# Kernel optimization log

Measured on AMD Instinct MI355X. Metric: run time of the kernel, lower is better.

The kernel has to match this reference:

```python
import jax, jax.numpy as jnp
import numpy as np

B, IN, CTRL, M, V, OUT = 2048, 64, 512, 1024, 64, 64


def setup_inputs() -> dict:
    key = jax.random.key(0)
    ks = jax.random.split(key, 20)
    s = 0.05  # small param scale for numerical stability

    def rn(k, shape, scale):
        return jax.random.normal(k, shape, dtype=jnp.float32) * scale

    return {
        # forward args
        "x": rn(ks[0], (B, IN), 1.0),
        "h_prev": rn(ks[1], (B, CTRL), 0.1),
        "c_prev": rn(ks[2], (B, CTRL), 0.1),
        "read_weights_prev": jax.nn.softmax(rn(ks[3], (B, M), 1.0), axis=1),
        # parameters
        "memory": rn(ks[4], (M, V), 1.0),
        "W_ih": rn(ks[5], (4 * CTRL, IN + V), s),
        "b_ih": rn(ks[6], (4 * CTRL,), s),
        "W_hh": rn(ks[7], (4 * CTRL, CTRL), s),
        "b_hh": rn(ks[8], (4 * CTRL,), s),
        "W_read": rn(ks[9], (M, CTRL), s),
        "b_read": rn(ks[10], (M,), s),
        "W_write": rn(ks[11], (M, CTRL), s),
        "b_write": rn(ks[12], (M,), s),
        "W_erase": rn(ks[13], (V, CTRL), s),
        "b_erase": rn(ks[14], (V,), s),
        "W_add": rn(ks[15], (V, CTRL), s),
        "b_add": rn(ks[16], (V,), s),
        "W_out": rn(ks[17], (OUT, CTRL + V), s),
        "b_out": rn(ks[18], (OUT,), s),
    }


def reference(x, h_prev, c_prev, read_weights_prev, memory,
              W_ih, b_ih, W_hh, b_hh,
              W_read, b_read, W_write, b_write,
              W_erase, b_erase, W_add, b_add,
              W_out, b_out):
    # read with previous weights on pre-write memory: [B,M] @ [M,V] -> [B,V]
    read_prev = read_weights_prev @ memory
    inp = jnp.concatenate([x, read_prev], axis=1)  # [B, IN+V]

    # LSTMCell (PyTorch gate order: i, f, g, o)
    gates = inp @ W_ih.T + b_ih + h_prev @ W_hh.T + b_hh  # [B, 4*CTRL]
    i, f, g, o = jnp.split(gates, 4, axis=1)
    i = jax.nn.sigmoid(i)
    f = jax.nn.sigmoid(f)
    g = jnp.tanh(g)
    o = jax.nn.sigmoid(o)
    c = f * c_prev + i * g
    h = o * jnp.tanh(c)

    # addressing + erase/add vectors
    read_w = jax.nn.softmax(h @ W_read.T + b_read, axis=1)    # [B,M]
    write_w = jax.nn.softmax(h @ W_write.T + b_write, axis=1)  # [B,M]
    erase = jax.nn.sigmoid(h @ W_erase.T + b_erase)            # [B,V]
    add = jnp.tanh(h @ W_add.T + b_add)                        # [B,V]

    # outer-product erase/add memory update: [B,M,V]
    w = write_w[:, :, None]
    mem_new = memory[None, :, :] * (1.0 - w * erase[:, None, :]) + w * add[:, None, :]

    # read with new weights on post-write memory
    read_new = jnp.einsum('bm,bmv->bv', read_w, mem_new)

    out = jnp.concatenate([h, read_new], axis=1) @ W_out.T + b_out  # [B,OUT]
    return out
```

## Files before the change

### kernel.cpp

```cpp
#include <hip/hip_runtime.h>
#include <hip/hip_bf16.h>


typedef unsigned short u16;
typedef __attribute__((ext_vector_type(8))) short bf16x8;
typedef __attribute__((ext_vector_type(4))) float f32x4;

#define MFMA_BF16(a, b, c) __builtin_amdgcn_mfma_f32_16x16x32_bf16((a), (b), (c), 0, 0, 0)
#define LDW 136

__device__ __forceinline__ void dma16(const void* g, void* l) {
    __builtin_amdgcn_global_load_lds(
        (const __attribute__((address_space(1))) unsigned int*)g,
        (__attribute__((address_space(3))) unsigned int*)l, 16, 0, 0);
}

__device__ __forceinline__ u16 f2bf(float f) {
    union { float f; unsigned int u; } a; a.f = f;
    return (u16)((a.u + 0x7FFFu + ((a.u >> 16) & 1u)) >> 16);
}

__device__ __forceinline__ void pack_store4(float a0, float a1, float a2, float a3, u16* d) {
    union { __hip_bfloat162 h[2]; uint2 u; } cv;
    cv.h[0] = __float22bfloat162_rn(make_float2(a0, a1));
    cv.h[1] = __float22bfloat162_rn(make_float2(a2, a3));
    *(uint2*)d = cv.u;
}

__device__ __forceinline__ void cvt4(const float* __restrict__ s, u16* __restrict__ d) {
    float4 v = *(const float4*)s;
    pack_store4(v.x, v.y, v.z, v.w, d);
}
// ... 44 lines not shown
    return r.u;
}

__device__ __forceinline__ float sigf(float x) { return 1.f / (1.f + __expf(-x)); }
__device__ __forceinline__ float fast_tanh(float x) { return 1.f - 2.f / (__expf(2.f * x) + 1.f); }

#define PIPE_BAR_PRE_CNT()  do {                                              \
    asm volatile("s_waitcnt vmcnt(6) lgkmcnt(0)" ::: "memory");               \
    __builtin_amdgcn_s_barrier();                                             \
    __builtin_amdgcn_sched_barrier(0);                                        \
} while (0)
#define PIPE_BAR_PRE_ZERO() do {                                              \
    asm volatile("s_waitcnt vmcnt(0) lgkmcnt(0)" ::: "memory");               \
    __builtin_amdgcn_s_barrier();                                             \
    __builtin_amdgcn_sched_barrier(0);                                        \
} while (0)
#define PIPE_BAR_POST() do {                                                  \
    __builtin_amdgcn_sched_barrier(0);                                        \
    asm volatile("s_waitcnt lgkmcnt(0)" ::: "memory");                        \
    __builtin_amdgcn_s_barrier();                                             \
    __builtin_amdgcn_sched_barrier(0);                                        \
} while (0)

__global__ __launch_bounds__(256) void k_pre(
    const float* __restrict__ x, const float* __restrict__ h_prev, const float* __restrict__ rwp,
    const float* __restrict__ memory, const float* __restrict__ W_ih, const float* __restrict__ W_hh,
    const float* __restrict__ W_read, const float* __restrict__ W_write, const float* __restrict__ W_erase,
    const float* __restrict__ W_add, const float* __restrict__ W_out,
    u16* x_t, u16* ht_t, u16* wcat_t, u16* Wcat2_t, u16* Wo_rn, u16* memt, float* rp)
{
    __shared__ u16 As[64 * LDW];
    __shared__ u16 Bs[64 * LDW];
    const int tid = threadIdx.x;

    if (blockIdx.x < 128) {
        const int mb = blockIdx.x & 31, ks = blockIdx.x >> 5;
        const int w = tid >> 6, lane = tid & 63;
        const int lrow = lane & 15, lq = lane >> 4;
        const int m0 = mb * 64, k0 = ks * 256;
        const int m_loc = tid >> 1, v0 = (tid & 1) * 32;
        f32x4 acc[4] = {};
        for (int kt = 0; kt < 2; ++kt) {
#pragma unroll
            for (int i = 0; i < 4; ++i) {
                int idx = i * 256 + tid, r = idx >> 4, c = (idx & 15) * 8;
                *(uint4*)(&As[r * LDW + c]) = cvt8u(rwp + (m0 + r) * 1024 + k0 + kt * 128 + c);
            }
#pragma unroll
            for (int j = 0; j < 8; ++j) {
                float4 q = *(const float4*)(memory + (k0 + kt * 128 + m_loc) * 64 + v0 + 4 * j);
                Bs[(v0 + 4 * j + 0) * LDW + m_loc] = f2bf(q.x);
                Bs[(v0 + 4 * j + 1) * LDW + m_loc] = f2bf(q.y);
                Bs[(v0 + 4 * j + 2) * LDW + m_loc] = f2bf(q.z);
                Bs[(v0 + 4 * j + 3) * LDW + m_loc] = f2bf(q.w);
            }
            __syncthreads();
#pragma unroll
            for (int kk = 0; kk < 128; kk += 32) {
                bf16x8 a  = *(const bf16x8*)(&As[(16 * w + lrow) * LDW + kk + 8 * lq]);
                bf16x8 b0 = *(const bf16x8*)(&Bs[(lrow) * LDW + kk + 8 * lq]);
                bf16x8 b1 = *(const bf16x8*)(&Bs[(16 + lrow) * LDW + kk + 8 * lq]);
                bf16x8 b2 = *(const bf16x8*)(&Bs[(32 + lrow) * LDW + kk + 8 * lq]);
                bf16x8 b3 = *(const bf16x8*)(&Bs[(48 + lrow) * LDW + kk + 8 * lq]);
                acc[0] = MFMA_BF16(a, b0, acc[0]);
                acc[1] = MFMA_BF16(a, b1, acc[1]);
                acc[2] = MFMA_BF16(a, b2, acc[2]);
                acc[3] = MFMA_BF16(a, b3, acc[3]);
            }
            __syncthreads();
        }
        float* rps = rp + ks * 131072;
#pragma unroll
        for (int nj = 0; nj < 4; ++nj)
#pragma unroll
            for (int r = 0; r < 4; ++r) {
                int row = m0 + 16 * w + 4 * lq + r, col = 16 * nj + lrow;
                rps[row * 64 + col] = acc[nj][r];
            }
        return;
    }

    int t = (blockIdx.x - 128) * 256 + tid;
    if (t < 32768) {
        int r = t >> 4, c = (t & 15) * 4;
        cvt4(x + r * 64 + c, x_t + ((r >> 7) * 8 + (c >> 3)) * 1024 + (r & 127) * 8 + (c & 7));
        return;
    }
    t -= 32768;
    if (t < 262144) {
        int r = t >> 7, c = (t & 127) * 4;
        cvt4(h_prev + r * 512 + c, ht_t + ((r >> 7) * 64 + (c >> 3)) * 1024 + (r & 127) * 8 + (c & 7));
        return;
    }
    t -= 262144;
    if (t < 65536) {
        int r = t >> 5, c = (t & 31) * 4;
        int g = r >> 9, j = r & 511;
        int bn = j >> 4, row64 = (g << 4) + (j & 15);
        int cd = (c < 64) ? c + 64 : c - 64;
        cvt4(W_ih + r * 128 + c, wcat_t + (bn * 5) * 8192 + (cd >> 3) * 512 + row64 * 8 + (cd & 7));
        return;
    }
    t -= 65536;
    if (t < 262144) {
        int r = t >> 7, c = (t & 127) * 4;
        int g = r >> 9, j = r & 511;
        int bn = j >> 4, row64 = (g << 4) + (j & 15);
        int cd = 128 + c;
        cvt4(W_hh + r * 512 + c, wcat_t + (bn * 5 + (cd >> 7)) * 8192 + ((cd >> 3) & 15) * 512 + row64 * 8 + (cd & 7));
        return;
    }
    t -= 262144;
    if (t < 131072) {
        int r = t >> 7, c = (t & 127) * 4;
        cvt4(W_read + t * 4, Wcat2_t + ((r >> 6) * 4 + (c >> 7)) * 8192 + ((c >> 3) & 15) * 512 + (r & 63) * 8 + (c & 7));
        return;
    }
    t -= 131072;
    if (t < 131072) {
        int r = t >> 7, c = (t & 127) * 4;
        cvt4(W_write + t * 4, Wcat2_t + ((16 + (r >> 6)) * 4 + (c >> 7)) * 8192 + ((c >> 3) & 15) * 512 + (r & 63) * 8 + (c & 7));
        return;
    }
    t -= 131072;
    if (t < 8192) {
        int r = t >> 7, c = (t & 127) * 4;
        cvt4(W_erase + t * 4, Wcat2_t + (32 * 4 + (c >> 7)) * 8192 + ((c >> 3) & 15) * 512 + r * 8 + (c & 7));
        return;
    }
    t -= 8192;
    if (t < 8192) {
        int r = t >> 7, c = (t & 127) * 4;
        cvt4(W_add + t * 4, Wcat2_t + (33 * 4 + (c >> 7)) * 8192 + ((c >> 3) & 15) * 512 + r * 8 + (c & 7));
        return;
    }
    t -= 8192;
    if (t < 9216) {
        int r = t / 144, c = (t % 144) * 4;
        if (c < 512)
            cvt4(W_out + r * 576 + c, Wcat2_t + (34 * 4 + (c >> 7)) * 8192 + ((c >> 3) & 15) * 512 + r * 8 + (c & 7));
        else
            cvt4(W_out + r * 576 + c, Wo_rn + r * 64 + (c - 512));
        return;
    }
    t -= 9216;
    if (t < 16384) {
        int v = t >> 8, m = (t & 255) * 4;
        pack_store4(memory[m * 64 + v], memory[(m + 1) * 64 + v],
                    memory[(m + 2) * 64 + v], memory[(m + 3) * 64 + v], memt + v * 1024 + m);
    }
}

__global__ __launch_bounds__(256) void k_gates(const u16* __restrict__ x_t, const u16* __restrict__ ht_t,
                                               const float* __restrict__ rp, const u16* __restrict__ wcat_t,
                                               const float* __restrict__ b_ih, const float* __restrict__ b_hh,
                                               const float* __restrict__ c_prev, u16* __restrict__ hrn_t)
{
    __shared__ u16 As[2][8192];
    __shared__ u16 Bs[2][4096];
    const int tid = threadIdx.x, w = tid >> 6, lane = tid & 63;
    const int lrow = lane & 15, lq = lane >> 4;
    const int mt = blockIdx.x, bn = blockIdx.y;
    const int m0 = mt * 128;
    f32x4 acc[2][4] = {};

#pragma unroll
    for (int i = 0; i < 4; ++i) {
        int cp = i * 256 + tid;
        *(uint4*)(&As[0][cp * 8]) = cvt8u_sum4(rp, (m0 + (cp & 127)) * 64 + (cp >> 7) * 8);
    }
#pragma unroll
    for (int i = 0; i < 2; ++i) {
        int cp = i * 256 + tid;
        dma16(wcat_t + (bn * 5) * 8192 + cp * 8, &Bs[0][(i * 256 + w * 64) * 8]);
    }

#pragma unroll
    for (int t = 0; t < 10; ++t) {
        if (t < 9) {
            const int tn = t + 1, b = tn & 1;
            const u16* asrc = (tn == 1) ? (x_t + mt * 8192)
                                        : (ht_t + mt * 65536 + (tn - 2) * 8192);
#pragma unroll
            for (int i = 0; i < 4; ++i) {
                int cp = i * 256 + tid;
                dma16(asrc + cp * 8, &As[b][(i * 256 + w * 64) * 8]);
            }
#pragma unroll
            for (int i = 0; i < 2; ++i) {
                int cp = i * 256 + tid;
                dma16(wcat_t + (bn * 5 + (tn >> 1)) * 8192 + (tn & 1) * 4096 + cp * 8,
                      &Bs[b][(i * 256 + w * 64) * 8]);
            }
            PIPE_BAR_PRE_CNT();
        } else {
            PIPE_BAR_PRE_ZERO();
        }
        const int b = t & 1;
#pragma unroll
        for (int kk = 0; kk < 64; kk += 32) {
            const int ob = (kk >> 3) + lq;
            bf16x8 a0 = *(const bf16x8*)(&As[b][ob * 1024 + (32 * w + lrow) * 8]);
            bf16x8 a1 = *(const bf16x8*)(&As[b][ob * 1024 + (32 * w + 16 + lrow) * 8]);
            bf16x8 b0 = *(const bf16x8*)(&Bs[b][ob * 512 + (lrow) * 8]);
            bf16x8 b1 = *(const bf16x8*)(&Bs[b][ob * 512 + (16 + lrow) * 8]);
            bf16x8 b2 = *(const bf16x8*)(&Bs[b][ob * 512 + (32 + lrow) * 8]);
            bf16x8 b3 = *(const bf16x8*)(&Bs[b][ob * 512 + (48 + lrow) * 8]);
            acc[0][0] = MFMA_BF16(a0, b0, acc[0][0]);
            acc[0][1] = MFMA_BF16(a0, b1, acc[0][1]);
            acc[0][2] = MFMA_BF16(a0, b2, acc[0][2]);
            acc[0][3] = MFMA_BF16(a0, b3, acc[0][3]);
            acc[1][0] = MFMA_BF16(a1, b0, acc[1][0]);
            acc[1][1] = MFMA_BF16(a1, b1, acc[1][1]);
            acc[1][2] = MFMA_BF16(a1, b2, acc[1][2]);
            acc[1][3] = MFMA_BF16(a1, b3, acc[1][3]);
        }
        PIPE_BAR_POST();
    }

    const int j = bn * 16 + lrow;
    const float bI = b_ih[j] + b_hh[j];
    const float bF = b_ih[512 + j] + b_hh[512 + j];
    const float bG = b_ih[1024 + j] + b_hh[1024 + j];
    const float bO = b_ih[1536 + j] + b_hh[1536 + j];
#pragma unroll
    for (int mi = 0; mi < 2; ++mi)
#pragma unroll
        for (int r = 0; r < 4; ++r) {
            int row = m0 + 32 * w + 16 * mi + 4 * lq + r;
            float ig = sigf(acc[mi][0][r] + bI);
            float fg = sigf(acc[mi][1][r] + bF);
            float gg = fast_tanh(acc[mi][2][r] + bG);
            float og = sigf(acc[mi][3][r] + bO);
            float c = fg * c_prev[row * 512 + j] + ig * gg;
            hrn_t[(row >> 7) * 65536 + (j >> 3) * 1024 + (row & 127) * 8 + (j & 7)] =
                f2bf(og * fast_tanh(c));
        }
}

__global__ __launch_bounds__(256) void k_heads(const u16* __restrict__ hrn_t, const u16* __restrict__ Wcat2_t,
                                               const float* __restrict__ b_read, const float* __restrict__ b_write,
                                               const float* __restrict__ b_erase, const float* __restrict__ b_add,
                                               const float* __restrict__ b_out,
                                               u16* __restrict__ pre_r, u16* __restrict__ pre_w,
                                               float* __restrict__ erase, float* __restrict__ add,
                                               float* __restrict__ out)
{
    __shared__ u16 As[2][8192];
    __shared__ u16 Bs[2][4096];
    const int tid = threadIdx.x, w = tid >> 6, lane = tid & 63;
    const int lrow = lane & 15, lq = lane >> 4;
    const int mt = blockIdx.x, bn = blockIdx.y;
    const int m0 = mt * 128;
    f32x4 acc[2][4] = {};

#pragma unroll
    for (int i = 0; i < 4; ++i) {
        int cp = i * 256 + tid;
        dma16(hrn_t + mt * 65536 + cp * 8, &As[0][(i * 256 + w * 64) * 8]);
    }
#pragma unroll
    for (int i = 0; i < 2; ++i) {
        int cp = i * 256 + tid;
        dma16(Wcat2_t + (bn * 4) * 8192 + cp * 8, &Bs[0][(i * 256 + w * 64) * 8]);
    }

#pragma unroll
    for (int t = 0; t < 8; ++t) {
        if (t < 7) {
            const int tn = t + 1, b = tn & 1;
#pragma unroll
            for (int i = 0; i < 4; ++i) {
                int cp = i * 256 + tid;
                dma16(hrn_t + mt * 65536 + tn * 8192 + cp * 8, &As[b][(i * 256 + w * 64) * 8]);
            }
#pragma unroll
            for (int i = 0; i < 2; ++i) {
                int cp = i * 256 + tid;
                dma16(Wcat2_t + (bn * 4 + (tn >> 1)) * 8192 + (tn & 1) * 4096 + cp * 8,
                      &Bs[b][(i * 256 + w * 64) * 8]);
            }
            PIPE_BAR_PRE_CNT();
        } else {
            PIPE_BAR_PRE_ZERO();
        }
        const int b = t & 1;
#pragma unroll
        for (int kk = 0; kk < 64; kk += 32) {
            const int ob = (kk >> 3) + lq;
            bf16x8 a0 = *(const bf16x8*)(&As[b][ob * 1024 + (32 * w + lrow) * 8]);
            bf16x8 a1 = *(const bf16x8*)(&As[b][ob * 1024 + (32 * w + 16 + lrow) * 8]);
            bf16x8 b0 = *(const bf16x8*)(&Bs[b][ob * 512 + (lrow) * 8]);
            bf16x8 b1 = *(const bf16x8*)(&Bs[b][ob * 512 + (16 + lrow) * 8]);
            bf16x8 b2 = *(const bf16x8*)(&Bs[b][ob * 512 + (32 + lrow) * 8]);
            bf16x8 b3 = *(const bf16x8*)(&Bs[b][ob * 512 + (48 + lrow) * 8]);
            acc[0][0] = MFMA_BF16(a0, b0, acc[0][0]);
            acc[0][1] = MFMA_BF16(a0, b1, acc[0][1]);
            acc[0][2] = MFMA_BF16(a0, b2, acc[0][2]);
            acc[0][3] = MFMA_BF16(a0, b3, acc[0][3]);
            acc[1][0] = MFMA_BF16(a1, b0, acc[1][0]);
            acc[1][1] = MFMA_BF16(a1, b1, acc[1][1]);
            acc[1][2] = MFMA_BF16(a1, b2, acc[1][2]);
            acc[1][3] = MFMA_BF16(a1, b3, acc[1][3]);
        }
        PIPE_BAR_POST();
    }

#pragma unroll
    for (int mi = 0; mi < 2; ++mi)
#pragma unroll
        for (int nj = 0; nj < 4; ++nj)
#pragma unroll
            for (int r = 0; r < 4; ++r) {
                int row = m0 + 32 * w + 16 * mi + 4 * lq + r;
                int col = bn * 64 + 16 * nj + lrow;
                float v = acc[mi][nj][r];
                if (bn < 16)       pre_r[row * 1024 + col] = f2bf(v + b_read[col]);
                else if (bn < 32)  pre_w[row * 1024 + (col - 1024)] = f2bf(v + b_write[col - 1024]);
                else if (bn == 32) erase[row * 64 + (col - 2048)] = sigf(v + b_erase[col - 2048]);
                else if (bn == 33) add[row * 64 + (col - 2112)] = fast_tanh(v + b_add[col - 2112]);
                else               out[row * 64 + (col - 2176)] = v + b_out[col - 2176];
            }
}

#define SLDW 520

__global__ __launch_bounds__(256) void k_tail(const u16* __restrict__ pre_r, const u16* __restrict__ pre_w,
                                              const u16* __restrict__ memt, const u16* __restrict__ Wo_rn,
                                              const float* __restrict__ erase, const float* __restrict__ add,
                                              float* __restrict__ out)
{
    __shared__ u16 rwS[16 * SLDW];
    __shared__ u16 rw2S[16 * SLDW];
    __shared__ u16 BsP[64 * LDW];
    __shared__ u16 Ps[16 * 72];
    __shared__ float s_sh[16];
    const int tid = threadIdx.x, w = tid >> 6, lane = tid & 63;
    const int lrow = lane & 15, lq = lane >> 4;
    const int mb = blockIdx.x >> 1, kh = blockIdx.x & 1;
    const int m0 = mb * 16, k0 = kh * 512;

    {
        const int row = tid >> 4, c16 = tid & 15;
        const int row_g = m0 + row;
        const u16* prp = pre_r + row_g * 1024;
        const u16* pwp = pre_w + row_g * 1024;
        float vr[64], vw[64];
#pragma unroll
        for (int q = 0; q < 8; ++q) {
            bfu4_to_f8(*(const uint4*)(prp + q * 128 + c16 * 8), vr + 8 * q);
            bfu4_to_f8(*(const uint4*)(pwp + q * 128 + c16 * 8), vw + 8 * q);
        }
        float mr = vr[0], mw = vw[0];
#pragma unroll
        for (int i = 1; i < 64; ++i) { mr = fmaxf(mr, vr[i]); mw = fmaxf(mw, vw[i]); }
#pragma unroll
        for (int o = 1; o < 16; o <<= 1) {
            mr = fmaxf(mr, __shfl_xor(mr, o, 64));
            mw = fmaxf(mw, __shfl_xor(mw, o, 64));
        }
        float sr = 0.f, sw = 0.f;
#pragma unroll
        for (int i = 0; i < 64; ++i) {
            vr[i] = __expf(vr[i] - mr); sr += vr[i];
            vw[i] = __expf(vw[i] - mw); sw += vw[i];
        }
#pragma unroll
        for (int o = 1; o < 16; o <<= 1) {
            sr += __shfl_xor(sr, o, 64);
            sw += __shfl_xor(sw, o, 64);
        }
        const float isr = 1.f / sr, isw = 1.f / sw;
        float ss = 0.f;
#pragma unroll
        for (int q = 0; q < 8; ++q) {
            float a8[8], r8[8];
#pragma unroll
            for (int i = 0; i < 8; ++i) {
                float a = vr[8 * q + i] * isr;
                float r2 = a * (vw[8 * q + i] * isw);
                a8[i] = a; r8[i] = r2;
                ss += r2;
            }
            if ((q >> 2) == kh) {
                int cb = (q - 4 * kh) * 128 + c16 * 8;
                *(uint4*)(&rwS[row * SLDW + cb])  = pack8(a8);
                *(uint4*)(&rw2S[row * SLDW + cb]) = pack8(r8);
            }
        }
#pragma unroll
        for (int o = 1; o < 16; o <<= 1) ss += __shfl_xor(ss, o, 64);
        if (c16 == 0) s_sh[row] = ss;
    }
    __syncthreads();

    f32x4 acc1 = {}, acc2 = {};
    for (int kt = 0; kt < 4; ++kt) {
#pragma unroll
        for (int i = 0; i < 4; ++i) {
            int idx = i * 256 + tid, r = idx >> 4, c = (idx & 15) * 8;
            *(uint4*)(&BsP[r * LDW + c]) = *(const uint4*)(memt + r * 1024 + k0 + kt * 128 + c);
        }
        __syncthreads();
#pragma unroll
        for (int kk = 0; kk < 128; kk += 32) {
            bf16x8 a1 = *(const bf16x8*)(&rwS[lrow * SLDW + kt * 128 + kk + 8 * lq]);
            bf16x8 a2 = *(const bf16x8*)(&rw2S[lrow * SLDW + kt * 128 + kk + 8 * lq]);
            bf16x8 b  = *(const bf16x8*)(&BsP[(16 * w + lrow) * LDW + kk + 8 * lq]);
            acc1 = MFMA_BF16(a1, b, acc1);
            acc2 = MFMA_BF16(a2, b, acc2);
        }
        __syncthreads();
    }

#pragma unroll
    for (int r = 0; r < 4; ++r) {
        int row_l = 4 * lq + r, col = 16 * w + lrow;
        int row_g = m0 + row_l;
        float p = acc1[r] - erase[row_g * 64 + col] * acc2[r];
        if (kh == 0) p += add[row_g * 64 + col] * s_sh[row_l];
        Ps[row_l * 72 + col] = f2bf(p);
    }
#pragma unroll
    for (int i = 0; i < 2; ++i) {
        int idx = i * 256 + tid, r = idx >> 3, c = (idx & 7) * 8;
        *(uint4*)(&BsP[r * LDW + c]) = *(const uint4*)(Wo_rn + r * 64 + c);
    }
    __syncthreads();

    f32x4 acc3 = {};
#pragma unroll
    for (int kk = 0; kk < 64; kk += 32) {
        bf16x8 a = *(const bf16x8*)(&Ps[lrow * 72 + kk + 8 * lq]);
        bf16x8 b = *(const bf16x8*)(&BsP[(16 * w + lrow) * LDW + kk + 8 * lq]);
        acc3 = MFMA_BF16(a, b, acc3);
    }
#pragma unroll
    for (int r = 0; r < 4; ++r) {
        int row_g = m0 + 4 * lq + r, col = 16 * w + lrow;
        atomicAdd(&out[row_g * 64 + col], acc3[r]);
    }
}

extern "C" void kernel_launch(void* const* d_in, const int* in_sizes, int n_in,
                              void* d_out, int out_size, void* d_ws, size_t ws_size,
                              hipStream_t stream)
{
    const float* x        = (const float*)d_in[0];
    const float* h_prev   = (const float*)d_in[1];
    const float* c_prev   = (const float*)d_in[2];
    const float* rwp      = (const float*)d_in[3];
    const float* memory   = (const float*)d_in[4];
    const float* W_ih     = (const float*)d_in[5];
    const float* b_ih     = (const float*)d_in[6];
    const float* W_hh     = (const float*)d_in[7];
    const float* b_hh     = (const float*)d_in[8];
    const float* W_read   = (const float*)d_in[9];
    const float* b_read   = (const float*)d_in[10];
    const float* W_write  = (const float*)d_in[11];
    const float* b_write  = (const float*)d_in[12];
    const float* W_erase  = (const float*)d_in[13];
    const float* b_erase  = (const float*)d_in[14];
    const float* W_add    = (const float*)d_in[15];
    const float* b_add    = (const float*)d_in[16];
    const float* W_out    = (const float*)d_in[17];
    const float* b_out    = (const float*)d_in[18];
    float* out = (float*)d_out;

    char* wsp = (char*)d_ws;
    u16*   x_t     = (u16*)(wsp + 0);
    u16*   ht_t    = (u16*)(wsp + 262144);
    u16*   wcat_t  = (u16*)(wsp + 2359296);
    u16*   memt    = (u16*)(wsp + 4980736);
    u16*   Wcat2_t = (u16*)(wsp + 5111808);
    u16*   Wo_rn   = (u16*)(wsp + 7405568);
    float* rp      = (float*)(wsp + 7413760);
    u16*   hrn_t   = (u16*)(wsp + 9510912);
    u16*   pre_r   = (u16*)(wsp + 11608064);
    u16*   pre_w   = (u16*)(wsp + 15802368);
    float* erase   = (float*)(wsp + 19996672);
    float* add     = (float*)(wsp + 20520960);

    k_pre<<<3748, 256, 0, stream>>>(x, h_prev, rwp, memory, W_ih, W_hh, W_read, W_write,
                                    W_erase, W_add, W_out,
                                    x_t, ht_t, wcat_t, Wcat2_t, Wo_rn, memt, rp);
    k_gates<<<dim3(16, 32), 256, 0, stream>>>(x_t, ht_t, rp, wcat_t, b_ih, b_hh, c_prev, hrn_t);
    k_heads<<<dim3(16, 35), 256, 0, stream>>>(hrn_t, Wcat2_t, b_read, b_write, b_erase, b_add, b_out,
                                              pre_r, pre_w, erase, add, out);
    k_tail<<<256, 256, 0, stream>>>(pre_r, pre_w, memt, Wo_rn, erase, add, out);
}
```

Baseline: 157.5 us.

## Fuse four kernels into one persistent kernel with software grid barriers

Merges the preprocessing, gate GEMM, head GEMM and tail stages into a single 512-block kernel. Stages are separated by atomic-counter grid barriers instead of kernel launch boundaries, and the conversion work is spread over a grid-stride loop. The goal is to remove launch overhead and the tail-drain gaps between kernels. In exchange, it relies on all 512 blocks being co-resident (launch bounds set to 2 blocks per CU) and adds spin-wait barrier costs. It also reduces parallelism for the conversion stage, which previously used 3748 blocks.

```diff
diff --git a/kernel.cpp b/kernel.cpp
--- a/kernel.cpp
+++ b/kernel.cpp
@@ -8,6 +8,25 @@
 
 #define MFMA_BF16(a, b, c) __builtin_amdgcn_mfma_f32_16x16x32_bf16((a), (b), (c), 0, 0, 0)
 #define LDW 136
+#define SLDW 520
+#define SMEM_BYTES 53248
+
+__device__ unsigned g_bar[3];
+
+__device__ __forceinline__ void grid_barrier(int idx) {
+    __syncthreads();
+    if (threadIdx.x == 0) {
+        __threadfence();
+        unsigned ticket = __hip_atomic_fetch_add(&g_bar[idx], 1u,
+                              __ATOMIC_ACQ_REL, __HIP_MEMORY_SCOPE_AGENT);
+        unsigned target = (ticket & ~511u) + 512u;
+        while (__hip_atomic_load(&g_bar[idx], __ATOMIC_RELAXED,
+                                 __HIP_MEMORY_SCOPE_AGENT) < target)
+            __builtin_amdgcn_s_sleep(8);
+    }
+    __syncthreads();
+    __threadfence();
+}
 
 __device__ __forceinline__ void dma16(const void* g, void* l) {
     __builtin_amdgcn_global_load_lds(
@@ -98,21 +117,119 @@
     __builtin_amdgcn_sched_barrier(0);                                        \
 } while (0)
 
-__global__ __launch_bounds__(256) void k_pre(
-    const float* __restrict__ x, const float* __restrict__ h_prev, const float* __restrict__ rwp,
-    const float* __restrict__ memory, const float* __restrict__ W_ih, const float* __restrict__ W_hh,
-    const float* __restrict__ W_read, const float* __restrict__ W_write, const float* __restrict__ W_erase,
-    const float* __restrict__ W_add, const float* __restrict__ W_out,
-    u16* x_t, u16* ht_t, u16* wcat_t, u16* Wcat2_t, u16* Wo_rn, u16* memt, float* rp)
+__device__ __forceinline__ void convert_unit(int t,
+    const float* __restrict__ x, const float* __restrict__ h_prev,
+    const float* __restrict__ W_ih, const float* __restrict__ W_hh,
+    const float* __restrict__ W_read, const float* __restrict__ W_write,
+    const float* __restrict__ W_erase, const float* __restrict__ W_add,
+    const float* __restrict__ W_out, const float* __restrict__ memory,
+    u16* x_t, u16* ht_t, u16* wcat_t, u16* Wcat2_t, u16* Wo_rn, u16* memt)
 {
-    __shared__ u16 As[64 * LDW];
-    __shared__ u16 Bs[64 * LDW];
-    const int tid = threadIdx.x;
-
-    if (blockIdx.x < 128) {
-        const int mb = blockIdx.x & 31, ks = blockIdx.x >> 5;
-        const int w = tid >> 6, lane = tid & 63;
-        const int lrow = lane & 15, lq = lane >> 4;
+    if (t < 32768) {
+        int r = t >> 4, c = (t & 15) * 4;
+        cvt4(x + r * 64 + c, x_t + ((r >> 7) * 8 + (c >> 3)) * 1024 + (r & 127) * 8 + (c & 7));
+        return;
+    }
+    t -= 32768;
+    if (t < 262144) {
+        int r = t >> 7, c = (t & 127) * 4;
+        cvt4(h_prev + r * 512 + c, ht_t + ((r >> 7) * 64 + (c >> 3)) * 1024 + (r & 127) * 8 + (c & 7));
+        return;
+    }
+    t -= 262144;
+    if (t < 65536) {
+        int r = t >> 5, c = (t & 31) * 4;
+        int g = r >> 9, j = r & 511;
+        int bn = j >> 4, row64 = (g << 4) + (j & 15);
+        int cd = (c < 64) ? c + 64 : c - 64;
+        cvt4(W_ih + r * 128 + c, wcat_t + (bn * 5) * 8192 + (cd >> 3) * 512 + row64 * 8 + (cd & 7));
+        return;
+    }
+    t -= 65536;
+    if (t < 262144) {
+        int r = t >> 7, c = (t & 127) * 4;
+        int g = r >> 9, j = r & 511;
+        int bn = j >> 4, row64 = (g << 4) + (j & 15);
+        int cd = 128 + c;
+        cvt4(W_hh + r * 512 + c, wcat_t + (bn * 5 + (cd >> 7)) * 8192 + ((cd >> 3) & 15) * 512 + row64 * 8 + (cd & 7));
+        return;
+    }
+    t -= 262144;
+    if (t < 131072) {
+        int r = t >> 7, c = (t & 127) * 4;
+        cvt4(W_read + t * 4, Wcat2_t + ((r >> 6) * 4 + (c >> 7)) * 8192 + ((c >> 3) & 15) * 512 + (r & 63) * 8 + (c & 7));
+        return;
+    }
+    t -= 131072;
+    if (t < 131072) {
+        int r = t >> 7, c = (t & 127) * 4;
+        cvt4(W_write + t * 4, Wcat2_t + ((16 + (r >> 6)) * 4 + (c >> 7)) * 8192 + ((c >> 3) & 15) * 512 + (r & 63) * 8 + (c & 7));
+        return;
+    }
+    t -= 131072;
+    if (t < 8192) {
+        int r = t >> 7, c = (t & 127) * 4;
+        cvt4(W_erase + t * 4, Wcat2_t + (32 * 4 + (c >> 7)) * 8192 + ((c >> 3) & 15) * 512 + r * 8 + (c & 7));
+        return;
+    }
+    t -= 8192;
+    if (t < 8192) {
+        int r = t >> 7, c = (t & 127) * 4;
+        cvt4(W_add + t * 4, Wcat2_t + (33 * 4 + (c >> 7)) * 8192 + ((c >> 3) & 15) * 512 + r * 8 + (c & 7));
+        return;
+    }
+    t -= 8192;
+    if (t < 9216) {
+        int r = t / 144, c = (t % 144) * 4;
+        if (c < 512)
+            cvt4(W_out + r * 576 + c, Wcat2_t + (34 * 4 + (c >> 7)) * 8192 + ((c >> 3) & 15) * 512 + r * 8 + (c & 7));
+        else
+            cvt4(W_out + r * 576 + c, Wo_rn + r * 64 + (c - 512));
+        return;
+    }
+    t -= 9216;
+    {
+        int v = t >> 8, m = (t & 255) * 4;
+        pack_store4(memory[m * 64 + v], memory[(m + 1) * 64 + v],
+                    memory[(m + 2) * 64 + v], memory[(m + 3) * 64 + v], memt + v * 1024 + m);
+    }
+}
+
+__global__ __launch_bounds__(256, 2) void k_fused(
+    const float* __restrict__ x, const float* __restrict__ h_prev, const float* __restrict__ c_prev,
+    const float* __restrict__ rwp, const float* __restrict__ memory,
+    const float* __restrict__ W_ih, const float* __restrict__ b_ih,
+    const float* __restrict__ W_hh, const float* __restrict__ b_hh,
+    const float* __restrict__ W_read, const float* __restrict__ b_read,
+    const float* __restrict__ W_write, const float* __restrict__ b_write,
+    const float* __restrict__ W_erase, const float* __restrict__ b_erase,
+    const float* __restrict__ W_add, const float* __restrict__ b_add,
+    const float* __restrict__ W_out, const float* __restrict__ b_out,
+    float* __restrict__ out, char* __restrict__ wsp)
+{
+    __shared__ __align__(16) char smem[SMEM_BYTES];
+
+    u16*   x_t     = (u16*)(wsp + 0);
+    u16*   ht_t    = (u16*)(wsp + 262144);
+    u16*   wcat_t  = (u16*)(wsp + 2359296);
+    u16*   memt    = (u16*)(wsp + 4980736);
+    u16*   Wcat2_t = (u16*)(wsp + 5111808);
+    u16*   Wo_rn   = (u16*)(wsp + 7405568);
+    float* rp      = (float*)(wsp + 7413760);
+    u16*   hrn_t   = (u16*)(wsp + 9510912);
+    u16*   pre_r   = (u16*)(wsp + 11608064);
+    u16*   pre_w   = (u16*)(wsp + 15802368);
+    float* erase   = (float*)(wsp + 19996672);
+    float* add     = (float*)(wsp + 20520960);
+
+    const int bid = blockIdx.x;
+    const int tid = threadIdx.x, w = tid >> 6, lane = tid & 63;
+    const int lrow = lane & 15, lq = lane >> 4;
+
+    if (bid < 128) {
+        u16* As = (u16*)smem;
+        u16* Bs = (u16*)(smem + 64 * LDW * 2);
+        const int mb = bid & 31, ks = bid >> 5;
         const int m0 = mb * 64, k0 = ks * 256;
         const int m_loc = tid >> 1, v0 = (tid & 1) * 32;
         f32x4 acc[4] = {};
@@ -153,368 +270,269 @@
                 int row = m0 + 16 * w + 4 * lq + r, col = 16 * nj + lrow;
                 rps[row * 64 + col] = acc[nj][r];
             }
-        return;
-    }
-
-    int t = (blockIdx.x - 128) * 256 + tid;
-    if (t < 32768) {
-        int r = t >> 4, c = (t & 15) * 4;
-        cvt4(x + r * 64 + c, x_t + ((r >> 7) * 8 + (c >> 3)) * 1024 + (r & 127) * 8 + (c & 7));
-        return;
-    }
-    t -= 32768;
-    if (t < 262144) {
-        int r = t >> 7, c = (t & 127) * 4;
-        cvt4(h_prev + r * 512 + c, ht_t + ((r >> 7) * 64 + (c >> 3)) * 1024 + (r & 127) * 8 + (c & 7));
-        return;
-    }
-    t -= 262144;
-    if (t < 65536) {
-        int r = t >> 5, c = (t & 31) * 4;
-        int g = r >> 9, j = r & 511;
-        int bn = j >> 4, row64 = (g << 4) + (j & 15);
-        int cd = (c < 64) ? c + 64 : c - 64;
-        cvt4(W_ih + r * 128 + c, wcat_t + (bn * 5) * 8192 + (cd >> 3) * 512 + row64 * 8 + (cd & 7));
-        return;
-    }
-    t -= 65536;
-    if (t < 262144) {
-        int r = t >> 7, c = (t & 127) * 4;
-        int g = r >> 9, j = r & 511;
-        int bn = j >> 4, row64 = (g << 4) + (j & 15);
-        int cd = 128 + c;
-        cvt4(W_hh + r * 512 + c, wcat_t + (bn * 5 + (cd >> 7)) * 8192 + ((cd >> 3) & 15) * 512 + row64 * 8 + (cd & 7));
-        return;
-    }
-    t -= 262144;
-    if (t < 131072) {
-        int r = t >> 7, c = (t & 127) * 4;
-        cvt4(W_read + t * 4, Wcat2_t + ((r >> 6) * 4 + (c >> 7)) * 8192 + ((c >> 3) & 15) * 512 + (r & 63) * 8 + (c & 7));
-        return;
-    }
-    t -= 131072;
-    if (t < 131072) {
-        int r = t >> 7, c = (t & 127) * 4;
-        cvt4(W_write + t * 4, Wcat2_t + ((16 + (r >> 6)) * 4 + (c >> 7)) * 8192 + ((c >> 3) & 15) * 512 + (r & 63) * 8 + (c & 7));
-        return;
-    }
-    t -= 131072;
-    if (t < 8192) {
-        int r = t >> 7, c = (t & 127) * 4;
-        cvt4(W_erase + t * 4, Wcat2_t + (32 * 4 + (c >> 7)) * 8192 + ((c >> 3) & 15) * 512 + r * 8 + (c & 7));
-        return;
-    }
-    t -= 8192;
-    if (t < 8192) {
-        int r = t >> 7, c = (t & 127) * 4;
-        cvt4(W_add + t * 4, Wcat2_t + (33 * 4 + (c >> 7)) * 8192 + ((c >> 3) & 15) * 512 + r * 8 + (c & 7));
-        return;
-    }
-    t -= 8192;
-    if (t < 9216) {
-        int r = t / 144, c = (t % 144) * 4;
-        if (c < 512)
-            cvt4(W_out + r * 576 + c, Wcat2_t + (34 * 4 + (c >> 7)) * 8192 + ((c >> 3) & 15) * 512 + r * 8 + (c & 7));
-        else
-            cvt4(W_out + r * 576 + c, Wo_rn + r * 64 + (c - 512));
-        return;
-    }
-    t -= 9216;
-    if (t < 16384) {
-        int v = t >> 8, m = (t & 255) * 4;
-        pack_store4(memory[m * 64 + v], memory[(m + 1) * 64 + v],
-                    memory[(m + 2) * 64 + v], memory[(m + 3) * 64 + v], memt + v * 1024 + m);
-    }
-}
-
-__global__ __launch_bounds__(256) void k_gates(const u16* __restrict__ x_t, const u16* __restrict__ ht_t,
-                                               const float* __restrict__ rp, const u16* __restrict__ wcat_t,
-                                               const float* __restrict__ b_ih, const float* __restrict__ b_hh,
-                                               const float* __restrict__ c_prev, u16* __restrict__ hrn_t)
-{
-    __shared__ u16 As[2][8192];
-    __shared__ u16 Bs[2][4096];
-    const int tid = threadIdx.x, w = tid >> 6, lane = tid & 63;
-    const int lrow = lane & 15, lq = lane >> 4;
-    const int mt = blockIdx.x, bn = blockIdx.y;
-    const int m0 = mt * 128;
-    f32x4 acc[2][4] = {};
-
-#pragma unroll
-    for (int i = 0; i < 4; ++i) {
-        int cp = i * 256 + tid;
-        *(uint4*)(&As[0][cp * 8]) = cvt8u_sum4(rp, (m0 + (cp & 127)) * 64 + (cp >> 7) * 8);
-    }
-#pragma unroll
-    for (int i = 0; i < 2; ++i) {
-        int cp = i * 256 + tid;
-        dma16(wcat_t + (bn * 5) * 8192 + cp * 8, &Bs[0][(i * 256 + w * 64) * 8]);
-    }
-
-#pragma unroll
-    for (int t = 0; t < 10; ++t) {
-        if (t < 9) {
-            const int tn = t + 1, b = tn & 1;
-            const u16* asrc = (tn == 1) ? (x_t + mt * 8192)
-                                        : (ht_t + mt * 65536 + (tn - 2) * 8192);
-#pragma unroll
-            for (int i = 0; i < 4; ++i) {
-                int cp = i * 256 + tid;
-                dma16(asrc + cp * 8, &As[b][(i * 256 + w * 64) * 8]);
-            }
-#pragma unroll
-            for (int i = 0; i < 2; ++i) {
-                int cp = i * 256 + tid;
-                dma16(wcat_t + (bn * 5 + (tn >> 1)) * 8192 + (tn & 1) * 4096 + cp * 8,
-                      &Bs[b][(i * 256 + w * 64) * 8]);
-            }
-            PIPE_BAR_PRE_CNT();
-        } else {
-            PIPE_BAR_PRE_ZERO();
-        }
-        const int b = t & 1;
-#pragma unroll
-        for (int kk = 0; kk < 64; kk += 32) {
-            const int ob = (kk >> 3) + lq;
-            bf16x8 a0 = *(const bf16x8*)(&As[b][ob * 1024 + (32 * w + lrow) * 8]);
-            bf16x8 a1 = *(const bf16x8*)(&As[b][ob * 1024 + (32 * w + 16 + lrow) * 8]);
-            bf16x8 b0 = *(const bf16x8*)(&Bs[b][ob * 512 + (lrow) * 8]);
-            bf16x8 b1 = *(const bf16x8*)(&Bs[b][ob * 512 + (16 + lrow) * 8]);
-            bf16x8 b2 = *(const bf16x8*)(&Bs[b][ob * 512 + (32 + lrow) * 8]);
-            bf16x8 b3 = *(const bf16x8*)(&Bs[b][ob * 512 + (48 + lrow) * 8]);
-            acc[0][0] = MFMA_BF16(a0, b0, acc[0][0]);
-            acc[0][1] = MFMA_BF16(a0, b1, acc[0][1]);
-            acc[0][2] = MFMA_BF16(a0, b2, acc[0][2]);
-            acc[0][3] = MFMA_BF16(a0, b3, acc[0][3]);
-            acc[1][0] = MFMA_BF16(a1, b0, acc[1][0]);
-            acc[1][1] = MFMA_BF16(a1, b1, acc[1][1]);
-            acc[1][2] = MFMA_BF16(a1, b2, acc[1][2]);
-            acc[1][3] = MFMA_BF16(a1, b3, acc[1][3]);
-        }
-        PIPE_BAR_POST();
-    }
-
-    const int j = bn * 16 + lrow;
-    const float bI = b_ih[j] + b_hh[j];
-    const float bF = b_ih[512 + j] + b_hh[512 + j];
-    const float bG = b_ih[1024 + j] + b_hh[1024 + j];
-    const float bO = b_ih[1536 + j] + b_hh[1536 + j];
-#pragma unroll
-    for (int mi = 0; mi < 2; ++mi)
-#pragma unroll
-        for (int r = 0; r < 4; ++r) {
-            int row = m0 + 32 * w + 16 * mi + 4 * lq + r;
-            float ig = sigf(acc[mi][0][r] + bI);
-            float fg = sigf(acc[mi][1][r] + bF);
-            float gg = fast_tanh(acc[mi][2][r] + bG);
-            float og = sigf(acc[mi][3][r] + bO);
-            float c = fg * c_prev[row * 512 + j] + ig * gg;
-            hrn_t[(row >> 7) * 65536 + (j >> 3) * 1024 + (row & 127) * 8 + (j & 7)] =
-                f2bf(og * fast_tanh(c));
-        }
-}
-
-__global__ __launch_bounds__(256) void k_heads(const u16* __restrict__ hrn_t, const u16* __restrict__ Wcat2_t,
-                                               const float* __restrict__ b_read, const float* __restrict__ b_write,
-                                               const float* __restrict__ b_erase, const float* __restrict__ b_add,
-                                               const float* __restrict__ b_out,
-                                               u16* __restrict__ pre_r, u16* __restrict__ pre_w,
-                                               float* __restrict__ erase, float* __restrict__ add,
-                                               float* __restrict__ out)
-{
-    __shared__ u16 As[2][8192];
-    __shared__ u16 Bs[2][4096];
-    const int tid = threadIdx.x, w = tid >> 6, lane = tid & 63;
-    const int lrow = lane & 15, lq = lane >> 4;
-    const int mt = blockIdx.x, bn = blockIdx.y;
-    const int m0 = mt * 128;
-    f32x4 acc[2][4] = {};
-
-#pragma unroll
-    for (int i = 0; i < 4; ++i) {
-        int cp = i * 256 + tid;
-        dma16(hrn_t + mt * 65536 + cp * 8, &As[0][(i * 256 + w * 64) * 8]);
-    }
-#pragma unroll
-    for (int i = 0; i < 2; ++i) {
-        int cp = i * 256 + tid;
-        dma16(Wcat2_t + (bn * 4) * 8192 + cp * 8, &Bs[0][(i * 256 + w * 64) * 8]);
-    }
-
-#pragma unroll
-    for (int t = 0; t < 8; ++t) {
-        if (t < 7) {
-            const int tn = t + 1, b = tn & 1;
-#pragma unroll
-            for (int i = 0; i < 4; ++i) {
-                int cp = i * 256 + tid;
-                dma16(hrn_t + mt * 65536 + tn * 8192 + cp * 8, &As[b][(i * 256 + w * 64) * 8]);
-            }
-#pragma unroll
-            for (int i = 0; i < 2; ++i) {
-                int cp = i * 256 + tid;
-                dma16(Wcat2_t + (bn * 4 + (tn >> 1)) * 8192 + (tn & 1) * 4096 + cp * 8,
-                      &Bs[b][(i * 256 + w * 64) * 8]);
-            }
-            PIPE_BAR_PRE_CNT();
-        } else {
-            PIPE_BAR_PRE_ZERO();
-        }
-        const int b = t & 1;
-#pragma unroll
-        for (int kk = 0; kk < 64; kk += 32) {
-            const int ob = (kk >> 3) + lq;
-            bf16x8 a0 = *(const bf16x8*)(&As[b][ob * 1024 + (32 * w + lrow) * 8]);
-            bf16x8 a1 = *(const bf16x8*)(&As[b][ob * 1024 + (32 * w + 16 + lrow) * 8]);
-            bf16x8 b0 = *(const bf16x8*)(&Bs[b][ob * 512 + (lrow) * 8]);
-            bf16x8 b1 = *(const bf16x8*)(&Bs[b][ob * 512 + (16 + lrow) * 8]);
-            bf16x8 b2 = *(const bf16x8*)(&Bs[b][ob * 512 + (32 + lrow) * 8]);
-            bf16x8 b3 = *(const bf16x8*)(&Bs[b][ob * 512 + (48 + lrow) * 8]);
-            acc[0][0] = MFMA_BF16(a0, b0, acc[0][0]);
-            acc[0][1] = MFMA_BF16(a0, b1, acc[0][1]);
-            acc[0][2] = MFMA_BF16(a0, b2, acc[0][2]);
-            acc[0][3] = MFMA_BF16(a0, b3, acc[0][3]);
-            acc[1][0] = MFMA_BF16(a1, b0, acc[1][0]);
-            acc[1][1] = MFMA_BF16(a1, b1, acc[1][1]);
-            acc[1][2] = MFMA_BF16(a1, b2, acc[1][2]);
-            acc[1][3] = MFMA_BF16(a1, b3, acc[1][3]);
-        }
-        PIPE_BAR_POST();
-    }
-
-#pragma unroll
-    for (int mi = 0; mi < 2; ++mi)
-#pragma unroll
-        for (int nj = 0; nj < 4; ++nj)
+    } else {
+        for (int t = (bid - 128) * 256 + tid; t < 926720; t += 384 * 256)
+            convert_unit(t, x, h_prev, W_ih, W_hh, W_read, W_write, W_erase, W_add,
+                         W_out, memory, x_t, ht_t, wcat_t, Wcat2_t, Wo_rn, memt);
+    }
+    grid_barrier(0);
+
+    {
+        u16* AsG = (u16*)smem;
+        u16* BsG = (u16*)(smem + 32768);
+        const int mt = bid & 15, bn = bid >> 4;
+        const int m0 = mt * 128;
+        f32x4 acc[2][4] = {};
+
+#pragma unroll
+        for (int i = 0; i < 4; ++i) {
+            int cp = i * 256 + tid;
+            *(uint4*)(&AsG[cp * 8]) = cvt8u_sum4(rp, (m0 + (cp & 127)) * 64 + (cp >> 7) * 8);
+        }
+#pragma unroll
+        for (int i = 0; i < 2; ++i) {
+            dma16(wcat_t + (bn * 5) * 8192 + (i * 256 + tid) * 8, &BsG[(i * 256 + w * 64) * 8]);
+        }
+
+#pragma unroll
+        for (int t = 0; t < 10; ++t) {
+            if (t < 9) {
+                const int tn = t + 1, b = tn & 1;
+                const u16* asrc = (tn == 1) ? (x_t + mt * 8192)
+                                            : (ht_t + mt * 65536 + (tn - 2) * 8192);
+#pragma unroll
+                for (int i = 0; i < 4; ++i)
+                    dma16(asrc + (i * 256 + tid) * 8, &AsG[b * 8192 + (i * 256 + w * 64) * 8]);
+#pragma unroll
+                for (int i = 0; i < 2; ++i)
+                    dma16(wcat_t + (bn * 5 + (tn >> 1)) * 8192 + (tn & 1) * 4096 + (i * 256 + tid) * 8,
+                          &BsG[b * 4096 + (i * 256 + w * 64) * 8]);
+                PIPE_BAR_PRE_CNT();
+            } else {
+                PIPE_BAR_PRE_ZERO();
+            }
+            const int b = t & 1;
+#pragma unroll
+            for (int kk = 0; kk < 64; kk += 32) {
+                const int ob = (kk >> 3) + lq;
+                bf16x8 a0 = *(const bf16x8*)(&AsG[b * 8192 + ob * 1024 + (32 * w + lrow) * 8]);
+                bf16x8 a1 = *(const bf16x8*)(&AsG[b * 8192 + ob * 1024 + (32 * w + 16 + lrow) * 8]);
+                bf16x8 b0 = *(const bf16x8*)(&BsG[b * 4096 + ob * 512 + (lrow) * 8]);
+                bf16x8 b1 = *(const bf16x8*)(&BsG[b * 4096 + ob * 512 + (16 + lrow) * 8]);
+                bf16x8 b2 = *(const bf16x8*)(&BsG[b * 4096 + ob * 512 + (32 + lrow) * 8]);
+                bf16x8 b3 = *(const bf16x8*)(&BsG[b * 4096 + ob * 512 + (48 + lrow) * 8]);
+                acc[0][0] = MFMA_BF16(a0, b0, acc[0][0]);
+                acc[0][1] = MFMA_BF16(a0, b1, acc[0][1]);
+                acc[0][2] = MFMA_BF16(a0, b2, acc[0][2]);
+                acc[0][3] = MFMA_BF16(a0, b3, acc[0][3]);
+                acc[1][0] = MFMA_BF16(a1, b0, acc[1][0]);
+                acc[1][1] = MFMA_BF16(a1, b1, acc[1][1]);
+                acc[1][2] = MFMA_BF16(a1, b2, acc[1][2]);
+                acc[1][3] = MFMA_BF16(a1, b3, acc[1][3]);
+            }
+            PIPE_BAR_POST();
+        }
+
+        const int j = bn * 16 + lrow;
+        const float bI = b_ih[j] + b_hh[j];
+        const float bF = b_ih[512 + j] + b_hh[512 + j];
+        const float bG = b_ih[1024 + j] + b_hh[1024 + j];
+        const float bO = b_ih[1536 + j] + b_hh[1536 + j];
+#pragma unroll
+        for (int mi = 0; mi < 2; ++mi)
 #pragma unroll
             for (int r = 0; r < 4; ++r) {
                 int row = m0 + 32 * w + 16 * mi + 4 * lq + r;
-                int col = bn * 64 + 16 * nj + lrow;
-                float v = acc[mi][nj][r];
-                if (bn < 16)       pre_r[row * 1024 + col] = f2bf(v + b_read[col]);
-                else if (bn < 32)  pre_w[row * 1024 + (col - 1024)] = f2bf(v + b_write[col - 1024]);
-                else if (bn == 32) erase[row * 64 + (col - 2048)] = sigf(v + b_erase[col - 2048]);
-                else if (bn == 33) add[row * 64 + (col - 2112)] = fast_tanh(v + b_add[col - 2112]);
-                else               out[row * 64 + (col - 2176)] = v + b_out[col - 2176];
-            }
-}
-
-#define SLDW 520
-
-__global__ __launch_bounds__(256) void k_tail(const u16* __restrict__ pre_r, const u16* __restrict__ pre_w,
-                                              const u16* __restrict__ memt, const u16* __restrict__ Wo_rn,
-                                              const float* __restrict__ erase, const float* __restrict__ add,
-                                              float* __restrict__ out)
-{
-    __shared__ u16 rwS[16 * SLDW];
-    __shared__ u16 rw2S[16 * SLDW];
-    __shared__ u16 BsP[64 * LDW];
-    __shared__ u16 Ps[16 * 72];
-    __shared__ float s_sh[16];
-    const int tid = threadIdx.x, w = tid >> 6, lane = tid & 63;
-    const int lrow = lane & 15, lq = lane >> 4;
-    const int mb = blockIdx.x >> 1, kh = blockIdx.x & 1;
-    const int m0 = mb * 16, k0 = kh * 512;
-
-    {
-        const int row = tid >> 4, c16 = tid & 15;
-        const int row_g = m0 + row;
-        const u16* prp = pre_r + row_g * 1024;
-        const u16* pwp = pre_w + row_g * 1024;
-        float vr[64], vw[64];
-#pragma unroll
-        for (int q = 0; q < 8; ++q) {
-            bfu4_to_f8(*(const uint4*)(prp + q * 128 + c16 * 8), vr + 8 * q);
-            bfu4_to_f8(*(const uint4*)(pwp + q * 128 + c16 * 8), vw + 8 * q);
-        }
-        float mr = vr[0], mw = vw[0];
-#pragma unroll
-        for (int i = 1; i < 64; ++i) { mr = fmaxf(mr, vr[i]); mw = fmaxf(mw, vw[i]); }
-#pragma unroll
-        for (int o = 1; o < 16; o <<= 1) {
-            mr = fmaxf(mr, __shfl_xor(mr, o, 64));
-            mw = fmaxf(mw, __shfl_xor(mw, o, 64));
-        }
-        float sr = 0.f, sw = 0.f;
-#pragma unroll
-        for (int i = 0; i < 64; ++i) {
-            vr[i] = __expf(vr[i] - mr); sr += vr[i];
-            vw[i] = __expf(vw[i] - mw); sw += vw[i];
-        }
-#pragma unroll
-        for (int o = 1; o < 16; o <<= 1) {
-            sr += __shfl_xor(sr, o, 64);
-            sw += __shfl_xor(sw, o, 64);
-        }
-        const float isr = 1.f / sr, isw = 1.f / sw;
-        float ss = 0.f;
-#pragma unroll
-        for (int q = 0; q < 8; ++q) {
-            float a8[8], r8[8];
-#pragma unroll
-            for (int i = 0; i < 8; ++i) {
-                float a = vr[8 * q + i] * isr;
-                float r2 = a * (vw[8 * q + i] * isw);
-                a8[i] = a; r8[i] = r2;
-                ss += r2;
-            }
-            if ((q >> 2) == kh) {
-                int cb = (q - 4 * kh) * 128 + c16 * 8;
-                *(uint4*)(&rwS[row * SLDW + cb])  = pack8(a8);
-                *(uint4*)(&rw2S[row * SLDW + cb]) = pack8(r8);
-            }
-        }
-#pragma unroll
-        for (int o = 1; o < 16; o <<= 1) ss += __shfl_xor(ss, o, 64);
-        if (c16 == 0) s_sh[row] = ss;
-    }
-    __syncthreads();
-
-    f32x4 acc1 = {}, acc2 = {};
-    for (int kt = 0; kt < 4; ++kt) {
-#pragma unroll
-        for (int i = 0; i < 4; ++i) {
-            int idx = i * 256 + tid, r = idx >> 4, c = (idx & 15) * 8;
-            *(uint4*)(&BsP[r * LDW + c]) = *(const uint4*)(memt + r * 1024 + k0 + kt * 128 + c);
+                float ig = sigf(acc[mi][0][r] + bI);
+                float fg = sigf(acc[mi][1][r] + bF);
+                float gg = fast_tanh(acc[mi][2][r] + bG);
+                float og = sigf(acc[mi][3][r] + bO);
+                float c = fg * c_prev[row * 512 + j] + ig * gg;
+                hrn_t[(row >> 7) * 65536 + (j >> 3) * 1024 + (row & 127) * 8 + (j & 7)] =
+                    f2bf(og * fast_tanh(c));
+            }
+    }
+    grid_barrier(1);
+
+    for (int tile = bid; tile < 560; tile += 512) {
+        u16* AsG = (u16*)smem;
+        u16* BsG = (u16*)(smem + 32768);
+        const int mt = tile & 15, bn = tile >> 4;
+        const int m0 = mt * 128;
+        f32x4 acc[2][4] = {};
+
+#pragma unroll
+        for (int i = 0; i < 4; ++i)
+            dma16(hrn_t + mt * 65536 + (i * 256 + tid) * 8, &AsG[(i * 256 + w * 64) * 8]);
+#pragma unroll
+        for (int i = 0; i < 2; ++i)
+            dma16(Wcat2_t + (bn * 4) * 8192 + (i * 256 + tid) * 8, &BsG[(i * 256 + w * 64) * 8]);
+
+#pragma unroll
+        for (int t = 0; t < 8; ++t) {
+            if (t < 7) {
+                const int tn = t + 1, b = tn & 1;
+#pragma unroll
+                for (int i = 0; i < 4; ++i)
+                    dma16(hrn_t + mt * 65536 + tn * 8192 + (i * 256 + tid) * 8,
+                          &AsG[b * 8192 + (i * 256 + w * 64) * 8]);
+#pragma unroll
+                for (int i = 0; i < 2; ++i)
+                    dma16(Wcat2_t + (bn * 4 + (tn >> 1)) * 8192 + (tn & 1) * 4096 + (i * 256 + tid) * 8,
+                          &BsG[b * 4096 + (i * 256 + w * 64) * 8]);
+                PIPE_BAR_PRE_CNT();
+            } else {
+                PIPE_BAR_PRE_ZERO();
+            }
+            const int b = t & 1;
+#pragma unroll
+            for (int kk = 0; kk < 64; kk += 32) {
+                const int ob = (kk >> 3) + lq;
+                bf16x8 a0 = *(const bf16x8*)(&AsG[b * 8192 + ob * 1024 + (32 * w + lrow) * 8]);
+                bf16x8 a1 = *(const bf16x8*)(&AsG[b * 8192 + ob * 1024 + (32 * w + 16 + lrow) * 8]);
+                bf16x8 b0 = *(const bf16x8*)(&BsG[b * 4096 + ob * 512 + (lrow) * 8]);
+                bf16x8 b1 = *(const bf16x8*)(&BsG[b * 4096 + ob * 512 + (16 + lrow) * 8]);
+                bf16x8 b2 = *(const bf16x8*)(&BsG[b * 4096 + ob * 512 + (32 + lrow) * 8]);
+                bf16x8 b3 = *(const bf16x8*)(&BsG[b * 4096 + ob * 512 + (48 + lrow) * 8]);
+                acc[0][0] = MFMA_BF16(a0, b0, acc[0][0]);
+                acc[0][1] = MFMA_BF16(a0, b1, acc[0][1]);
+                acc[0][2] = MFMA_BF16(a0, b2, acc[0][2]);
+                acc[0][3] = MFMA_BF16(a0, b3, acc[0][3]);
+                acc[1][0] = MFMA_BF16(a1, b0, acc[1][0]);
+                acc[1][1] = MFMA_BF16(a1, b1, acc[1][1]);
+                acc[1][2] = MFMA_BF16(a1, b2, acc[1][2]);
+                acc[1][3] = MFMA_BF16(a1, b3, acc[1][3]);
+            }
+            PIPE_BAR_POST();
+        }
+
+#pragma unroll
+        for (int mi = 0; mi < 2; ++mi)
+#pragma unroll
+            for (int nj = 0; nj < 4; ++nj)
+#pragma unroll
+                for (int r = 0; r < 4; ++r) {
+                    int row = m0 + 32 * w + 16 * mi + 4 * lq + r;
+                    int col = bn * 64 + 16 * nj + lrow;
+                    float v = acc[mi][nj][r];
+                    if (bn < 16)       pre_r[row * 1024 + col] = f2bf(v + b_read[col]);
+                    else if (bn < 32)  pre_w[row * 1024 + (col - 1024)] = f2bf(v + b_write[col - 1024]);
+                    else if (bn == 32) erase[row * 64 + (col - 2048)] = sigf(v + b_erase[col - 2048]);
+                    else if (bn == 33) add[row * 64 + (col - 2112)] = fast_tanh(v + b_add[col - 2112]);
+                    else               out[row * 64 + (col - 2176)] = v + b_out[col - 2176];
+                }
+    }
+    grid_barrier(2);
+
+    if (bid < 256) {
+        u16*   rwS  = (u16*)smem;
+        u16*   rw2S = (u16*)(smem + 16640);
+        u16*   BsP  = (u16*)(smem + 33280);
+        u16*   Ps   = (u16*)(smem + 50688);
+        float* s_sh = (float*)(smem + 52992);
+        const int mb = bid >> 1, kh = bid & 1;
+        const int m0 = mb * 16, k0 = kh * 512;
+
+        {
+            const int row = tid >> 4, c16 = tid & 15;
+            const int row_g = m0 + row;
+            const u16* prp = pre_r + row_g * 1024;
+            const u16* pwp = pre_w + row_g * 1024;
+            float vr[64], vw[64];
+#pragma unroll
+            for (int q = 0; q < 8; ++q) {
+                bfu4_to_f8(*(const uint4*)(prp + q * 128 + c16 * 8), vr + 8 * q);
+                bfu4_to_f8(*(const uint4*)(pwp + q * 128 + c16 * 8), vw + 8 * q);
+            }
+            float mr = vr[0], mw = vw[0];
+#pragma unroll
+            for (int i = 1; i < 64; ++i) { mr = fmaxf(mr, vr[i]); mw = fmaxf(mw, vw[i]); }
+#pragma unroll
+            for (int o = 1; o < 16; o <<= 1) {
+                mr = fmaxf(mr, __shfl_xor(mr, o, 64));
+                mw = fmaxf(mw, __shfl_xor(mw, o, 64));
+            }
+            float sr = 0.f, sw = 0.f;
+#pragma unroll
+            for (int i = 0; i < 64; ++i) {
+                vr[i] = __expf(vr[i] - mr); sr += vr[i];
+                vw[i] = __expf(vw[i] - mw); sw += vw[i];
+            }
+#pragma unroll
+            for (int o = 1; o < 16; o <<= 1) {
+                sr += __shfl_xor(sr, o, 64);
+                sw += __shfl_xor(sw, o, 64);
+            }
+            const float isr = 1.f / sr, isw = 1.f / sw;
+            float ss = 0.f;
+#pragma unroll
+            for (int q = 0; q < 8; ++q) {
+                float a8[8], r8[8];
+#pragma unroll
+                for (int i = 0; i < 8; ++i) {
+                    float a = vr[8 * q + i] * isr;
+                    float r2 = a * (vw[8 * q + i] * isw);
+                    a8[i] = a; r8[i] = r2;
+                    ss += r2;
+                }
+                if ((q >> 2) == kh) {
+                    int cb = (q - 4 * kh) * 128 + c16 * 8;
+                    *(uint4*)(&rwS[row * SLDW + cb])  = pack8(a8);
+                    *(uint4*)(&rw2S[row * SLDW + cb]) = pack8(r8);
+                }
+            }
+#pragma unroll
+            for (int o = 1; o < 16; o <<= 1) ss += __shfl_xor(ss, o, 64);
+            if (c16 == 0) s_sh[row] = ss;
         }
         __syncthreads();
-#pragma unroll
-        for (int kk = 0; kk < 128; kk += 32) {
-            bf16x8 a1 = *(const bf16x8*)(&rwS[lrow * SLDW + kt * 128 + kk + 8 * lq]);
-            bf16x8 a2 = *(const bf16x8*)(&rw2S[lrow * SLDW + kt * 128 + kk + 8 * lq]);
-            bf16x8 b  = *(const bf16x8*)(&BsP[(16 * w + lrow) * LDW + kk + 8 * lq]);
-            acc1 = MFMA_BF16(a1, b, acc1);
-            acc2 = MFMA_BF16(a2, b, acc2);
+
+        f32x4 acc1 = {}, acc2 = {};
+        for (int kt = 0; kt < 4; ++kt) {
+#pragma unroll
+            for (int i = 0; i < 4; ++i) {
+                int idx = i * 256 + tid, r = idx >> 4, c = (idx & 15) * 8;
+                *(uint4*)(&BsP[r * LDW + c]) = *(const uint4*)(memt + r * 1024 + k0 + kt * 128 + c);
+            }
+            __syncthreads();
+#pragma unroll
+            for (int kk = 0; kk < 128; kk += 32) {
+                bf16x8 a1 = *(const bf16x8*)(&rwS[lrow * SLDW + kt * 128 + kk + 8 * lq]);
+                bf16x8 a2 = *(const bf16x8*)(&rw2S[lrow * SLDW + kt * 128 + kk + 8 * lq]);
+                bf16x8 b  = *(const bf16x8*)(&BsP[(16 * w + lrow) * LDW + kk + 8 * lq]);
+                acc1 = MFMA_BF16(a1, b, acc1);
+                acc2 = MFMA_BF16(a2, b, acc2);
+            }
+            __syncthreads();
+        }
+
+#pragma unroll
+        for (int r = 0; r < 4; ++r) {
+            int row_l = 4 * lq + r, col = 16 * w + lrow;
+            int row_g = m0 + row_l;
+            float p = acc1[r] - erase[row_g * 64 + col] * acc2[r];
+            if (kh == 0) p += add[row_g * 64 + col] * s_sh[row_l];
+            Ps[row_l * 72 + col] = f2bf(p);
+        }
+#pragma unroll
+        for (int i = 0; i < 2; ++i) {
+            int idx = i * 256 + tid, r = idx >> 3, c = (idx & 7) * 8;
+            *(uint4*)(&BsP[r * LDW + c]) = *(const uint4*)(Wo_rn + r * 64 + c);
         }
         __syncthreads();
-    }
-
-#pragma unroll
-    for (int r = 0; r < 4; ++r) {
-        int row_l = 4 * lq + r, col = 16 * w + lrow;
-        int row_g = m0 + row_l;
-        float p = acc1[r] - erase[row_g * 64 + col] * acc2[r];
-        if (kh == 0) p += add[row_g * 64 + col] * s_sh[row_l];
-        Ps[row_l * 72 + col] = f2bf(p);
-    }
-#pragma unroll
-    for (int i = 0; i < 2; ++i) {
-        int idx = i * 256 + tid, r = idx >> 3, c = (idx & 7) * 8;
-        *(uint4*)(&BsP[r * LDW + c]) = *(const uint4*)(Wo_rn + r * 64 + c);
-    }
-    __syncthreads();
-
-    f32x4 acc3 = {};
-#pragma unroll
-    for (int kk = 0; kk < 64; kk += 32) {
-        bf16x8 a = *(const bf16x8*)(&Ps[lrow * 72 + kk + 8 * lq]);
-        bf16x8 b = *(const bf16x8*)(&BsP[(16 * w + lrow) * LDW + kk + 8 * lq]);
-        acc3 = MFMA_BF16(a, b, acc3);
-    }
-#pragma unroll
-    for (int r = 0; r < 4; ++r) {
-        int row_g = m0 + 4 * lq + r, col = 16 * w + lrow;
-        atomicAdd(&out[row_g * 64 + col], acc3[r]);
+
+        f32x4 acc3 = {};
+#pragma unroll
+        for (int kk = 0; kk < 64; kk += 32) {
+            bf16x8 a = *(const bf16x8*)(&Ps[lrow * 72 + kk + 8 * lq]);
+            bf16x8 b = *(const bf16x8*)(&BsP[(16 * w + lrow) * LDW + kk + 8 * lq]);
+            acc3 = MFMA_BF16(a, b, acc3);
+        }
+#pragma unroll
+        for (int r = 0; r < 4; ++r) {
+            int row_g = m0 + 4 * lq + r, col = 16 * w + lrow;
+            atomicAdd(&out[row_g * 64 + col], acc3[r]);
+        }
     }
 }
 
@@ -542,26 +560,10 @@
     const float* W_out    = (const float*)d_in[17];
     const float* b_out    = (const float*)d_in[18];
     float* out = (float*)d_out;
-
     char* wsp = (char*)d_ws;
-    u16*   x_t     = (u16*)(wsp + 0);
-    u16*   ht_t    = (u16*)(wsp + 262144);
-    u16*   wcat_t  = (u16*)(wsp + 2359296);
-    u16*   memt    = (u16*)(wsp + 4980736);
-    u16*   Wcat2_t = (u16*)(wsp + 5111808);
-    u16*   Wo_rn   = (u16*)(wsp + 7405568);
-    float* rp      = (float*)(wsp + 7413760);
-    u16*   hrn_t   = (u16*)(wsp + 9510912);
-    u16*   pre_r   = (u16*)(wsp + 11608064);
-    u16*   pre_w   = (u16*)(wsp + 15802368);
-    float* erase   = (float*)(wsp + 19996672);
-    float* add     = (float*)(wsp + 20520960);
-
-    k_pre<<<3748, 256, 0, stream>>>(x, h_prev, rwp, memory, W_ih, W_hh, W_read, W_write,
-                                    W_erase, W_add, W_out,
-                                    x_t, ht_t, wcat_t, Wcat2_t, Wo_rn, memt, rp);
-    k_gates<<<dim3(16, 32), 256, 0, stream>>>(x_t, ht_t, rp, wcat_t, b_ih, b_hh, c_prev, hrn_t);
-    k_heads<<<dim3(16, 35), 256, 0, stream>>>(hrn_t, Wcat2_t, b_read, b_write, b_erase, b_add, b_out,
-                                              pre_r, pre_w, erase, add, out);
-    k_tail<<<256, 256, 0, stream>>>(pre_r, pre_w, memt, Wo_rn, erase, add, out);
-}
+
+    k_fused<<<dim3(512), dim3(256), 0, stream>>>(
+        x, h_prev, c_prev, rwp, memory, W_ih, b_ih, W_hh, b_hh,
+        W_read, b_read, W_write, b_write, W_erase, b_erase, W_add, b_add,
+        W_out, b_out, out, wsp);
+}
```

After: 418.1 us. 2.65x slower.
